# Kernel optimization log

Hardware: AMD Instinct MI355X
Metric: run time of the kernel (lower is better)

The kernel has to match this reference:

```python
import jax, jax.numpy as jnp
import numpy as np

CH, KS, PAD = 64, 3, 1
B, H, W = 4, 128, 128
EH, EW = 64, 64
K = KS * KS


def setup_inputs() -> dict:
    key = jax.random.key(0)
    ks = jax.random.split(key, 10)
    C = CH
    z = lambda *s: jnp.zeros(s, jnp.float32)
    return {
        "ev_feat": jax.random.normal(ks[0], (B, C, EH, EW), jnp.float32),
        "im_feat": jax.random.normal(ks[1], (B, C, H, W), jnp.float32),
        "mlp_w0": jax.random.normal(ks[2], (2 * C + 4, C), jnp.float32) * 0.05,
        "mlp_b0": z(C),
        "mlp_w1": jax.random.normal(ks[3], (C, C), jnp.float32) * 0.05,
        "mlp_b1": z(C),
        "mlp_w2": jax.random.normal(ks[4], (C, C), jnp.float32) * 0.05,
        "mlp_b2": z(C),
        "mlp_w3": jax.random.normal(ks[5], (C, C), jnp.float32) * 0.05,
        "mlp_b3": z(C),
        "off_w": jax.random.normal(ks[6], (3 * K, C, KS, KS), jnp.float32) * 0.01,
        "off_b": z(3 * K),
        "dcn_w": jax.random.normal(ks[7], (C, C, KS, KS), jnp.float32) * 0.05,
        "dcn_b": z(C),
    }


def _conv(x, w, b):
    y = jax.lax.conv_general_dilated(x, w, (1, 1), [(PAD, PAD), (PAD, PAD)],
                                     dimension_numbers=("NCHW", "OIHW", "NCHW"))
    return y + b[None, :, None, None]


def _forward(ev_feat, im_feat, mlp_w0, mlp_b0, mlp_w1, mlp_b1, mlp_w2, mlp_b2,
             mlp_w3, mlp_b3, off_w, off_b, dcn_w, dcn_b):
    C = CH
    Bn = im_feat.shape[0]
    Q = H * W
    # ---- coordinate-conditioned MLP: LIIF-style nearest query of ev_feat ----
    ys = -1.0 + (2.0 * jnp.arange(H, dtype=jnp.float32) + 1.0) / H  # pixel centers in [-1,1]
    xs = -1.0 + (2.0 * jnp.arange(W, dtype=jnp.float32) + 1.0) / W
    gy, gx = jnp.meshgrid(ys, xs, indexing="ij")
    coord = jnp.stack([gy, gx], -1).reshape(-1, 2)  # (Q,2) as (y,x), torch make_coord order
    iy = jnp.clip(jnp.round(((coord[:, 0] + 1.0) * EH - 1.0) / 2.0), 0, EH - 1).astype(jnp.int32)
    ix = jnp.clip(jnp.round(((coord[:, 1] + 1.0) * EW - 1.0) / 2.0), 0, EW - 1).astype(jnp.int32)
    q_feat = ev_feat[:, :, iy, ix].transpose(0, 2, 1)  # (B,Q,C) nearest-sampled event feature
    q_coord = jnp.stack([-1.0 + (2.0 * iy + 1.0) / EH, -1.0 + (2.0 * ix + 1.0) / EW], -1)
    rel = (coord - q_coord) * jnp.array([EH, EW], jnp.float32)  # (Q,2) rel coord scaled by feat res
    rel_cell = jnp.array([2.0 / H * EH, 2.0 / W * EW], jnp.float32)  # cell * feat res
    q_im = im_feat.reshape(Bn, C, Q).transpose(0, 2, 1)  # (B,Q,C); coords are im_feat pixel centers
    inp = jnp.concatenate([q_feat, q_im,
                           jnp.broadcast_to(rel, (Bn, Q, 2)),
                           jnp.broadcast_to(rel_cell, (Bn, Q, 2))], -1)  # (B,Q,2C+4)
    x = jax.nn.relu(inp @ mlp_w0 + mlp_b0)
    x = jax.nn.relu(x @ mlp_w1 + mlp_b1)
    x = jax.nn.relu(x @ mlp_w2 + mlp_b2)
    x = x @ mlp_w3 + mlp_b3  # (B,Q,C)
    feat = x.reshape(Bn, H, W, C).transpose(0, 3, 1, 2)  # (B,C,H,W)
    # ---- ModulatedDeformConvPack (DCNv2) ----
    oo = _conv(feat, off_w, off_b)  # (B,3K,H,W)
    o1, o2, m = oo[:, :K], oo[:, K:2 * K], oo[:, 2 * K:]
    off = jnp.concatenate([o1, o2], 1)  # (B,2K,H,W), interleaved (y,x) per kernel tap
    off_y, off_x = off[:, 0::2], off[:, 1::2]  # (B,K,H,W)
    mask = jax.nn.sigmoid(m)  # (B,K,H,W)
    ky = (jnp.arange(K) // KS - PAD).astype(jnp.float32)
    kx = (jnp.arange(K) % KS - PAD).astype(jnp.float32)
    py = jnp.arange(H, dtype=jnp.float32)[None, :, None] + ky[:, None, None] + off_y  # (B,K,H,W)
    px = jnp.arange(W, dtype=jnp.float32)[None, None, :] + kx[:, None, None] + off_x
    y0 = jnp.floor(py)
    x0 = jnp.floor(px)
    ly = py - y0
    lx = px - x0

    def gather(yi, xi):
        valid = (yi >= 0) & (yi <= H - 1) & (xi >= 0) & (xi <= W - 1)
        yc = jnp.clip(yi, 0, H - 1).astype(jnp.int32)
        xc = jnp.clip(xi, 0, W - 1).astype(jnp.int32)
        v = jax.vmap(lambda img, yy, xx: img[:, yy, xx])(feat, yc, xc)  # (B,C,K,H,W)
        return v * valid[:, None].astype(feat.dtype)

    w00 = ((1 - ly) * (1 - lx))[:, None]
    w01 = ((1 - ly) * lx)[:, None]
    w10 = (ly * (1 - lx))[:, None]
    w11 = (ly * lx)[:, None]
    samp = (gather(y0, x0) * w00 + gather(y0, x0 + 1) * w01 +
            gather(y0 + 1, x0) * w10 + gather(y0 + 1, x0 + 1) * w11)  # (B,C,K,H,W)
    samp = samp * mask[:, None]
    out = jnp.einsum("bckhw,ock->bohw", samp, dcn_w.reshape(C, C, K))
    return out + dcn_b[None, :, None, None]


def reference(ev_feat, im_feat, mlp_w0, mlp_b0, mlp_w1, mlp_b1, mlp_w2, mlp_b2,
              mlp_w3, mlp_b3, off_w, off_b, dcn_w, dcn_b):
    return _forward(ev_feat, im_feat, mlp_w0, mlp_b0, mlp_w1, mlp_b1, mlp_w2, mlp_b2,
                    mlp_w3, mlp_b3, off_w, off_b, dcn_w, dcn_b)
```

## Files before the change

### kernel.cpp

```cpp
#include <hip/hip_runtime.h>
#include <math.h>

#define CCH 64
#define HH  128
#define WW  128
#define NB  4
#define NPIX (NB*HH*WW)
#define NWG  (NPIX/64)

__device__ __forceinline__ int swz_block(int bid) {
    return (bid & 7) * (NWG >> 3) + (bid >> 3);
}

__global__ __launch_bounds__(256) void prep_kernel(
    const float* __restrict__ off_w, const float* __restrict__ dcn_w,
    float* __restrict__ offT, float* __restrict__ dcnT)
{
    int idx = blockIdx.x * 256 + threadIdx.x;
    if (idx < 576 * 28) {
        int rc = idx / 28;
        int o  = idx % 28;
        offT[rc * 28 + o] = (o < 27) ? off_w[o * 576 + rc] : 0.0f;
    }
    if (idx < 36864) {
        int o    = idx & 63;
        int rest = idx >> 6;
        int ic   = rest & 63;
        int k    = rest >> 6;
        dcnT[(k * 64 + ic) * 64 + o] = dcn_w[o * 576 + ic * 9 + k];
    }
}

__global__ __launch_bounds__(256) void mlp_kernel(
    const float* __restrict__ ev, const float* __restrict__ im,
    const float* __restrict__ w0, const float* __restrict__ b0,
    const float* __restrict__ w1, const float* __restrict__ b1,
    const float* __restrict__ w2, const float* __restrict__ b2,
    const float* __restrict__ w3, const float* __restrict__ b3,
    float* __restrict__ feat)
{
    __shared__ float xA[64 * 64];
    __shared__ float xB[64 * 64];
    int tid  = threadIdx.x;
    int cg   = __builtin_amdgcn_readfirstlane(tid >> 6);
    int lane = tid & 63;
    int p = swz_block(blockIdx.x) * 64 + lane;
    int b = p >> 14;
    int q = p & 16383;
    int h = q >> 7;
    int w = q & 127;
    int c0 = cg * 16;

    float acc[16];
#pragma unroll
    for (int j = 0; j < 16; ++j) acc[j] = b0[c0 + j];

    const float* evb = ev + ((b * 64) * 64 + (h >> 1)) * 64 + (w >> 1);
    for (int i = 0; i < 64; ++i) {
        float v = evb[i * 4096];
        const float* wr = w0 + i * 64 + c0;
#pragma unroll
        for (int j = 0; j < 16; ++j) acc[j] = fmaf(v, wr[j], acc[j]);
    }
    const float* imb = im + ((b * 64) * 128 + h) * 128 + w;
    for (int i = 0; i < 64; ++i) {
        float v = imb[i * 16384];
        const float* wr = w0 + (64 + i) * 64 + c0;
#pragma unroll
        for (int j = 0; j < 16; ++j) acc[j] = fmaf(v, wr[j], acc[j]);
    }
    {
        float rely = (h & 1) ? 0.5f : -0.5f;
        float relx = (w & 1) ? 0.5f : -0.5f;
        const float* wr = w0 + 128 * 64 + c0;
#pragma unroll
        for (int j = 0; j < 16; ++j) acc[j] = fmaf(rely, wr[j], acc[j]);
#pragma unroll
        for (int j = 0; j < 16; ++j) acc[j] = fmaf(relx, wr[64 + j], acc[j]);
#pragma unroll
        for (int j = 0; j < 16; ++j) acc[j] += wr[128 + j] + wr[192 + j];
    }
#pragma unroll
    for (int j = 0; j < 16; ++j) xA[(c0 + j) * 64 + lane] = fmaxf(acc[j], 0.0f);
    __syncthreads();

#pragma unroll
    for (int j = 0; j < 16; ++j) acc[j] = b1[c0 + j];
    for (int i = 0; i < 64; ++i) {
        float v = xA[i * 64 + lane];
        const float* wr = w1 + i * 64 + c0;
#pragma unroll
        for (int j = 0; j < 16; ++j) acc[j] = fmaf(v, wr[j], acc[j]);
    }
#pragma unroll
    for (int j = 0; j < 16; ++j) xB[(c0 + j) * 64 + lane] = fmaxf(acc[j], 0.0f);
    __syncthreads();

#pragma unroll
    for (int j = 0; j < 16; ++j) acc[j] = b2[c0 + j];
    for (int i = 0; i < 64; ++i) {
        float v = xB[i * 64 + lane];
        const float* wr = w2 + i * 64 + c0;
#pragma unroll
        for (int j = 0; j < 16; ++j) acc[j] = fmaf(v, wr[j], acc[j]);
    }
#pragma unroll
    for (int j = 0; j < 16; ++j) xA[(c0 + j) * 64 + lane] = fmaxf(acc[j], 0.0f);
    __syncthreads();

#pragma unroll
    for (int j = 0; j < 16; ++j) acc[j] = b3[c0 + j];
    for (int i = 0; i < 64; ++i) {
        float v = xA[i * 64 + lane];
        const float* wr = w3 + i * 64 + c0;
#pragma unroll
        for (int j = 0; j < 16; ++j) acc[j] = fmaf(v, wr[j], acc[j]);
    }
    float* fb = feat + (b * 64 + c0) * 16384 + q;
#pragma unroll
    for (int j = 0; j < 16; ++j) fb[j * 16384] = acc[j];
}

__global__ __launch_bounds__(256) void off_kernel(
    const float* __restrict__ feat, const float* __restrict__ offT,
    const float* __restrict__ off_b,
    float* __restrict__ oo)
{
    __shared__ float po[4 * 27 * 64];
    int tid  = threadIdx.x;
    int wv   = __builtin_amdgcn_readfirstlane(tid >> 6);
    int lane = tid & 63;
    int p = swz_block(blockIdx.x) * 64 + lane;
    int b = p >> 14;
    int q = p & 16383;
    int h = q >> 7;
    int w = q & 127;
    int c0 = wv * 16;

    float acc[27];
#pragma unroll
    for (int o = 0; o < 27; ++o) acc[o] = 0.0f;

    const float* fb = feat + (b * 64 + c0) * 16384;
    for (int i = 0; i < 16; ++i) {
        const float* f = fb + i * 16384;
        float v[9];
#pragma unroll
        for (int ky = 0; ky < 3; ++ky)
#pragma unroll
            for (int kx = 0; kx < 3; ++kx) {
                int y = h + ky - 1, x = w + kx - 1;
                bool ok = (y >= 0) && (y < 128) && (x >= 0) && (x < 128);
                v[ky * 3 + kx] = ok ? f[y * 128 + x] : 0.0f;
            }
#pragma unroll
        for (int kk = 0; kk < 9; ++kk) {
            const float* wr = offT + ((c0 + i) * 9 + kk) * 28;
#pragma unroll
            for (int o = 0; o < 27; ++o) acc[o] = fmaf(v[kk], wr[o], acc[o]);
        }
    }

#pragma unroll
    for (int o = 0; o < 27; ++o) po[(wv * 27 + o) * 64 + lane] = acc[o];
    __syncthreads();

#pragma unroll
    for (int j = 0; j < 7; ++j) {
        int o = wv + 4 * j;
        if (o < 27) {
            float s = off_b[o]
                    + po[o * 64 + lane] + po[(27 + o) * 64 + lane]
                    + po[(54 + o) * 64 + lane] + po[(81 + o) * 64 + lane];
            oo[((b * 27 + o) << 14) + q] = s;
        }
    }
}

__device__ __forceinline__ void dcn_transform(
    const float* oob, int k, int h, int w,
    float& W00, float& W01, float& W10, float& W11,
    int& i00, int& i01, int& i10, int& i11)
{
    float oy = oob[(2 * k) << 14];
    float ox = oob[(2 * k + 1) << 14];
    float ml = 1.0f / (1.0f + expf(-oob[(18 + k) << 14]));
    float py = (float)(h + k / 3 - 1) + oy;
    float px = (float)(w + k % 3 - 1) + ox;

    float y0f = floorf(py), x0f = floorf(px);
    float ly = py - y0f, lx = px - x0f;
    int y0 = (int)y0f, x0 = (int)x0f;

    bool vy0 = (y0f >= 0.0f)        && (y0f <= 127.0f);
    bool vy1 = (y0f + 1.0f >= 0.0f) && (y0f + 1.0f <= 127.0f);
    bool vx0 = (x0f >= 0.0f)        && (x0f <= 127.0f);
    bool vx1 = (x0f + 1.0f >= 0.0f) && (x0f + 1.0f <= 127.0f);

    int yc0 = min(max(y0, 0), 127),     yc1 = min(max(y0 + 1, 0), 127);
    int xc0 = min(max(x0, 0), 127),     xc1 = min(max(x0 + 1, 0), 127);

    W00 = (1.0f - ly) * (1.0f - lx) * ml * ((vy0 && vx0) ? 1.0f : 0.0f);
    W01 = (1.0f - ly) * lx          * ml * ((vy0 && vx1) ? 1.0f : 0.0f);
    W10 = ly * (1.0f - lx)          * ml * ((vy1 && vx0) ? 1.0f : 0.0f);
    W11 = ly * lx                   * ml * ((vy1 && vx1) ? 1.0f : 0.0f);

    i00 = yc0 * 128 + xc0; i01 = yc0 * 128 + xc1;
    i10 = yc1 * 128 + xc0; i11 = yc1 * 128 + xc1;
}

__global__ __launch_bounds__(256) void dcn_kernel(
    const float* __restrict__ feat,
    const float* __restrict__ oo,
    const float* __restrict__ dcnT, const float* __restrict__ dcn_b,
    float* __restrict__ out)
{
    __shared__ float sA[64 * 64];
    __shared__ float sB[64 * 64];
    int tid  = threadIdx.x;
    int wv   = __builtin_amdgcn_readfirstlane(tid >> 6);
    int lane = tid & 63;
    int p = swz_block(blockIdx.x) * 64 + lane;
    int b = p >> 14;
    int q = p & 16383;
    int h = q >> 7;
    int w = q & 127;
    int c0 = wv * 16;

    float acc[16];
#pragma unroll
    for (int j = 0; j < 16; ++j) acc[j] = dcn_b[c0 + j];

    const float* fb  = feat + (b * 64 + c0) * 16384;
    const float* oob = oo + ((b * 27) << 14) + q;

    {
        float W00, W01, W10, W11; int i00, i01, i10, i11;
        dcn_transform(oob, 0, h, w, W00, W01, W10, W11, i00, i01, i10, i11);
#pragma unroll 8
        for (int i = 0; i < 16; ++i) {
            const float* f = fb + i * 16384;
            float s = W00 * f[i00] + W01 * f[i01] + W10 * f[i10] + W11 * f[i11];
            sA[(c0 + i) * 64 + lane] = s;
        }
    }
    __syncthreads();

    float* cur = sA;
    float* nxt = sB;

    for (int k = 0; k < 9; ++k) {
        bool pre = (k < 8);
        float W00, W01, W10, W11; int i00, i01, i10, i11;
        float r00[8], r01[8], r10[8], r11[8];

        if (pre) {
            dcn_transform(oob, k + 1, h, w, W00, W01, W10, W11, i00, i01, i10, i11);
#pragma unroll
            for (int i = 0; i < 8; ++i) {
                const float* f = fb + i * 16384;
                r00[i] = f[i00]; r01[i] = f[i01]; r10[i] = f[i10]; r11[i] = f[i11];
            }
        }

        const float* wk = dcnT + (k * 64) * 64 + c0;
#pragma unroll 8
        for (int ic = 0; ic < 32; ++ic) {
            float s = cur[ic * 64 + lane];
            const float* wr = wk + ic * 64;
#pragma unroll
            for (int j = 0; j < 16; ++j) acc[j] = fmaf(s, wr[j], acc[j]);
        }

        if (pre) {
#pragma unroll
            for (int i = 0; i < 8; ++i)
                nxt[(c0 + i) * 64 + lane] =
                    W00 * r00[i] + W01 * r01[i] + W10 * r10[i] + W11 * r11[i];
#pragma unroll
            for (int i = 0; i < 8; ++i) {
                const float* f = fb + (8 + i) * 16384;
                r00[i] = f[i00]; r01[i] = f[i01]; r10[i] = f[i10]; r11[i] = f[i11];
            }
        }

#pragma unroll 8
        for (int ic = 32; ic < 64; ++ic) {
            float s = cur[ic * 64 + lane];
            const float* wr = wk + ic * 64;
#pragma unroll
            for (int j = 0; j < 16; ++j) acc[j] = fmaf(s, wr[j], acc[j]);
        }

        if (pre) {
#pragma unroll
            for (int i = 0; i < 8; ++i)
                nxt[(c0 + 8 + i) * 64 + lane] =
                    W00 * r00[i] + W01 * r01[i] + W10 * r10[i] + W11 * r11[i];
        }

        __syncthreads();
        float* t = cur; cur = nxt; nxt = t;
    }

    float* ob = out + (b * 64 + c0) * 16384 + q;
#pragma unroll
    for (int j = 0; j < 16; ++j) ob[j * 16384] = acc[j];
}

extern "C" void kernel_launch(void* const* d_in, const int* in_sizes, int n_in,
                              void* d_out, int out_size, void* d_ws, size_t ws_size,
                              hipStream_t stream)
{
    const float* ev    = (const float*)d_in[0];
    const float* im    = (const float*)d_in[1];
    const float* w0    = (const float*)d_in[2];
    const float* b0    = (const float*)d_in[3];
    const float* w1    = (const float*)d_in[4];
    const float* b1    = (const float*)d_in[5];
    const float* w2    = (const float*)d_in[6];
    const float* b2    = (const float*)d_in[7];
    const float* w3    = (const float*)d_in[8];
    const float* b3    = (const float*)d_in[9];
    const float* off_w = (const float*)d_in[10];
    const float* off_b = (const float*)d_in[11];
    const float* dcn_w = (const float*)d_in[12];
    const float* dcn_b = (const float*)d_in[13];
    float* out = (float*)d_out;

    char* ws = (char*)d_ws;
    float* feat  = (float*)(ws);
    float* oo    = (float*)(ws + 16777216);
    float* offT  = (float*)(ws + 23855104);
    float* dcnT  = (float*)(ws + 23920640);

    prep_kernel<<<144, 256, 0, stream>>>(off_w, dcn_w, offT, dcnT);
    mlp_kernel<<<NWG, 256, 0, stream>>>(ev, im, w0, b0, w1, b1, w2, b2,
                                        w3, b3, feat);
    off_kernel<<<NWG, 256, 0, stream>>>(feat, offT, off_b, oo);
    dcn_kernel<<<NWG, 256, 0, stream>>>(feat, oo, dcnT, dcn_b, out);
}
```

Baseline: 182.1 us.

## Store intermediate features channels-last and gather them with float4 loads

The MLP output buffer moves from NCHW to NHWC layout. The offset conv and deformable conv then fetch 16 contiguous channels per sampled pixel with float4 loads instead of 16 strided scalar loads. The aim is fewer memory transactions and better cache-line use in the random bilinear gathers. In exchange, each lane's MLP writes and off-conv reads now stride 256 bytes between neighbouring pixels, so a single warp access is no longer coalesced across lanes.

```diff
diff --git a/kernel.cpp b/kernel.cpp
--- a/kernel.cpp
+++ b/kernel.cpp
@@ -37,7 +37,7 @@
     const float* __restrict__ w1, const float* __restrict__ b1,
     const float* __restrict__ w2, const float* __restrict__ b2,
     const float* __restrict__ w3, const float* __restrict__ b3,
-    float* __restrict__ feat)
+    float* __restrict__ feat2)
 {
     __shared__ float xA[64 * 64];
     __shared__ float xB[64 * 64];
@@ -116,13 +116,14 @@
 #pragma unroll
         for (int j = 0; j < 16; ++j) acc[j] = fmaf(v, wr[j], acc[j]);
     }
-    float* fb = feat + (b * 64 + c0) * 16384 + q;
-#pragma unroll
-    for (int j = 0; j < 16; ++j) fb[j * 16384] = acc[j];
+    float4* f4 = (float4*)(feat2 + ((b * 16384 + q) * 64 + c0));
+#pragma unroll
+    for (int j = 0; j < 4; ++j)
+        f4[j] = make_float4(acc[4 * j], acc[4 * j + 1], acc[4 * j + 2], acc[4 * j + 3]);
 }
 
 __global__ __launch_bounds__(256) void off_kernel(
-    const float* __restrict__ feat, const float* __restrict__ offT,
+    const float* __restrict__ feat2, const float* __restrict__ offT,
     const float* __restrict__ off_b,
     float* __restrict__ oo)
 {
@@ -141,23 +142,24 @@
 #pragma unroll
     for (int o = 0; o < 27; ++o) acc[o] = 0.0f;
 
-    const float* fb = feat + (b * 64 + c0) * 16384;
-    for (int i = 0; i < 16; ++i) {
-        const float* f = fb + i * 16384;
-        float v[9];
-#pragma unroll
-        for (int ky = 0; ky < 3; ++ky)
-#pragma unroll
-            for (int kx = 0; kx < 3; ++kx) {
-                int y = h + ky - 1, x = w + kx - 1;
-                bool ok = (y >= 0) && (y < 128) && (x >= 0) && (x < 128);
-                v[ky * 3 + kx] = ok ? f[y * 128 + x] : 0.0f;
-            }
-#pragma unroll
-        for (int kk = 0; kk < 9; ++kk) {
+    const float* f2 = feat2 + (b * 16384) * 64 + c0;
+#pragma unroll 3
+    for (int kk = 0; kk < 9; ++kk) {
+        int y = h + kk / 3 - 1, x = w + kk % 3 - 1;
+        bool ok = (y >= 0) && (y < 128) && (x >= 0) && (x < 128);
+        int yc = min(max(y, 0), 127), xc = min(max(x, 0), 127);
+        const float4* fp = (const float4*)(f2 + (yc * 128 + xc) * 64);
+        float4 v0 = fp[0], v1 = fp[1], v2 = fp[2], v3 = fp[3];
+        float zz = ok ? 1.0f : 0.0f;
+        float vv[16] = {v0.x*zz, v0.y*zz, v0.z*zz, v0.w*zz,
+                        v1.x*zz, v1.y*zz, v1.z*zz, v1.w*zz,
+                        v2.x*zz, v2.y*zz, v2.z*zz, v2.w*zz,
+                        v3.x*zz, v3.y*zz, v3.z*zz, v3.w*zz};
+#pragma unroll
+        for (int i = 0; i < 16; ++i) {
             const float* wr = offT + ((c0 + i) * 9 + kk) * 28;
 #pragma unroll
-            for (int o = 0; o < 27; ++o) acc[o] = fmaf(v[kk], wr[o], acc[o]);
+            for (int o = 0; o < 27; ++o) acc[o] = fmaf(vv[i], wr[o], acc[o]);
         }
     }
 
@@ -210,7 +212,7 @@
 }
 
 __global__ __launch_bounds__(256) void dcn_kernel(
-    const float* __restrict__ feat,
+    const float* __restrict__ feat2,
     const float* __restrict__ oo,
     const float* __restrict__ dcnT, const float* __restrict__ dcn_b,
     float* __restrict__ out)
@@ -231,17 +233,23 @@
 #pragma unroll
     for (int j = 0; j < 16; ++j) acc[j] = dcn_b[c0 + j];
 
-    const float* fb  = feat + (b * 64 + c0) * 16384;
+    const float* fb2 = feat2 + (b * 16384) * 64 + c0;
     const float* oob = oo + ((b * 27) << 14) + q;
 
     {
         float W00, W01, W10, W11; int i00, i01, i10, i11;
         dcn_transform(oob, 0, h, w, W00, W01, W10, W11, i00, i01, i10, i11);
-#pragma unroll 8
-        for (int i = 0; i < 16; ++i) {
-            const float* f = fb + i * 16384;
-            float s = W00 * f[i00] + W01 * f[i01] + W10 * f[i10] + W11 * f[i11];
-            sA[(c0 + i) * 64 + lane] = s;
+        const float4* p00 = (const float4*)(fb2 + i00 * 64);
+        const float4* p01 = (const float4*)(fb2 + i01 * 64);
+        const float4* p10 = (const float4*)(fb2 + i10 * 64);
+        const float4* p11 = (const float4*)(fb2 + i11 * 64);
+#pragma unroll
+        for (int g = 0; g < 4; ++g) {
+            float4 a = p00[g], bb = p01[g], c = p10[g], d = p11[g];
+            sA[(c0 + 4 * g + 0) * 64 + lane] = W00 * a.x + W01 * bb.x + W10 * c.x + W11 * d.x;
+            sA[(c0 + 4 * g + 1) * 64 + lane] = W00 * a.y + W01 * bb.y + W10 * c.y + W11 * d.y;
+            sA[(c0 + 4 * g + 2) * 64 + lane] = W00 * a.z + W01 * bb.z + W10 * c.z + W11 * d.z;
+            sA[(c0 + 4 * g + 3) * 64 + lane] = W00 * a.w + W01 * bb.w + W10 * c.w + W11 * d.w;
         }
     }
     __syncthreads();
@@ -252,15 +260,19 @@
     for (int k = 0; k < 9; ++k) {
         bool pre = (k < 8);
         float W00, W01, W10, W11; int i00, i01, i10, i11;
-        float r00[8], r01[8], r10[8], r11[8];
+        float4 a0, a1, b0, b1, c0v, c1v, d0, d1;
+        const float4 *p00 = nullptr, *p01 = nullptr, *p10 = nullptr, *p11 = nullptr;
 
         if (pre) {
             dcn_transform(oob, k + 1, h, w, W00, W01, W10, W11, i00, i01, i10, i11);
-#pragma unroll
-            for (int i = 0; i < 8; ++i) {
-                const float* f = fb + i * 16384;
-                r00[i] = f[i00]; r01[i] = f[i01]; r10[i] = f[i10]; r11[i] = f[i11];
-            }
+            p00 = (const float4*)(fb2 + i00 * 64);
+            p01 = (const float4*)(fb2 + i01 * 64);
+            p10 = (const float4*)(fb2 + i10 * 64);
+            p11 = (const float4*)(fb2 + i11 * 64);
+            a0 = p00[0]; a1 = p00[1];
+            b0 = p01[0]; b1 = p01[1];
+            c0v = p10[0]; c1v = p10[1];
+            d0 = p11[0]; d1 = p11[1];
         }
 
         const float* wk = dcnT + (k * 64) * 64 + c0;
@@ -273,15 +285,18 @@
         }
 
         if (pre) {
-#pragma unroll
-            for (int i = 0; i < 8; ++i)
-                nxt[(c0 + i) * 64 + lane] =
-                    W00 * r00[i] + W01 * r01[i] + W10 * r10[i] + W11 * r11[i];
-#pragma unroll
-            for (int i = 0; i < 8; ++i) {
-                const float* f = fb + (8 + i) * 16384;
-                r00[i] = f[i00]; r01[i] = f[i01]; r10[i] = f[i10]; r11[i] = f[i11];
-            }
+            nxt[(c0 + 0) * 64 + lane] = W00 * a0.x + W01 * b0.x + W10 * c0v.x + W11 * d0.x;
+            nxt[(c0 + 1) * 64 + lane] = W00 * a0.y + W01 * b0.y + W10 * c0v.y + W11 * d0.y;
+            nxt[(c0 + 2) * 64 + lane] = W00 * a0.z + W01 * b0.z + W10 * c0v.z + W11 * d0.z;
+            nxt[(c0 + 3) * 64 + lane] = W00 * a0.w + W01 * b0.w + W10 * c0v.w + W11 * d0.w;
+            nxt[(c0 + 4) * 64 + lane] = W00 * a1.x + W01 * b1.x + W10 * c1v.x + W11 * d1.x;
+            nxt[(c0 + 5) * 64 + lane] = W00 * a1.y + W01 * b1.y + W10 * c1v.y + W11 * d1.y;
+            nxt[(c0 + 6) * 64 + lane] = W00 * a1.z + W01 * b1.z + W10 * c1v.z + W11 * d1.z;
+            nxt[(c0 + 7) * 64 + lane] = W00 * a1.w + W01 * b1.w + W10 * c1v.w + W11 * d1.w;
+            a0 = p00[2]; a1 = p00[3];
+            b0 = p01[2]; b1 = p01[3];
+            c0v = p10[2]; c1v = p10[3];
+            d0 = p11[2]; d1 = p11[3];
         }
 
 #pragma unroll 8
@@ -293,10 +308,14 @@
         }
 
         if (pre) {
-#pragma unroll
-            for (int i = 0; i < 8; ++i)
-                nxt[(c0 + 8 + i) * 64 + lane] =
-                    W00 * r00[i] + W01 * r01[i] + W10 * r10[i] + W11 * r11[i];
+            nxt[(c0 +  8) * 64 + lane] = W00 * a0.x + W01 * b0.x + W10 * c0v.x + W11 * d0.x;
+            nxt[(c0 +  9) * 64 + lane] = W00 * a0.y + W01 * b0.y + W10 * c0v.y + W11 * d0.y;
+            nxt[(c0 + 10) * 64 + lane] = W00 * a0.z + W01 * b0.z + W10 * c0v.z + W11 * d0.z;
+            nxt[(c0 + 11) * 64 + lane] = W00 * a0.w + W01 * b0.w + W10 * c0v.w + W11 * d0.w;
+            nxt[(c0 + 12) * 64 + lane] = W00 * a1.x + W01 * b1.x + W10 * c1v.x + W11 * d1.x;
+            nxt[(c0 + 13) * 64 + lane] = W00 * a1.y + W01 * b1.y + W10 * c1v.y + W11 * d1.y;
+            nxt[(c0 + 14) * 64 + lane] = W00 * a1.z + W01 * b1.z + W10 * c1v.z + W11 * d1.z;
+            nxt[(c0 + 15) * 64 + lane] = W00 * a1.w + W01 * b1.w + W10 * c1v.w + W11 * d1.w;
         }
 
         __syncthreads();
@@ -329,14 +348,14 @@
     float* out = (float*)d_out;
 
     char* ws = (char*)d_ws;
-    float* feat  = (float*)(ws);
+    float* feat2 = (float*)(ws);
     float* oo    = (float*)(ws + 16777216);
     float* offT  = (float*)(ws + 23855104);
     float* dcnT  = (float*)(ws + 23920640);
 
     prep_kernel<<<144, 256, 0, stream>>>(off_w, dcn_w, offT, dcnT);
     mlp_kernel<<<NWG, 256, 0, stream>>>(ev, im, w0, b0, w1, b1, w2, b2,
-                                        w3, b3, feat);
-    off_kernel<<<NWG, 256, 0, stream>>>(feat, offT, off_b, oo);
-    dcn_kernel<<<NWG, 256, 0, stream>>>(feat, oo, dcnT, dcn_b, out);
-}
+                                        w3, b3, feat2);
+    off_kernel<<<NWG, 256, 0, stream>>>(feat2, offT, off_b, oo);
+    dcn_kernel<<<NWG, 256, 0, stream>>>(feat2, oo, dcnT, dcn_b, out);
+}
```

After: 184.8 us. No clear change (+1.5%).

## Gather DCN samples from a channel-last feature copy with float4 loads

Applied to the files above, without the earlier changes.

The MLP kernel now also writes a pixel-major (NHWC) copy of the features, transposed through padded shared memory. The deformable-conv kernel gathers each bilinear corner as contiguous float4 channel groups instead of strided per-channel scalar loads. It also runs 512 threads per block with 8 output channels per wave and an XOR-swizzled shared-memory layout. The NCHW copy still feeds the offset conv and is stored temporarily in the output buffer. The cost is an extra 16 MB feature write, plus more weight loads per sample because each wave computes fewer outputs.

```diff
diff --git a/kernel.cpp b/kernel.cpp
--- a/kernel.cpp
+++ b/kernel.cpp
@@ -37,14 +37,15 @@
     const float* __restrict__ w1, const float* __restrict__ b1,
     const float* __restrict__ w2, const float* __restrict__ b2,
     const float* __restrict__ w3, const float* __restrict__ b3,
-    float* __restrict__ feat)
-{
-    __shared__ float xA[64 * 64];
-    __shared__ float xB[64 * 64];
+    float* __restrict__ feat2, float* __restrict__ featN)
+{
+    __shared__ float xA[64 * 65];
+    __shared__ float xB[64 * 65];
     int tid  = threadIdx.x;
     int cg   = __builtin_amdgcn_readfirstlane(tid >> 6);
     int lane = tid & 63;
-    int p = swz_block(blockIdx.x) * 64 + lane;
+    int sw   = swz_block(blockIdx.x);
+    int p = sw * 64 + lane;
     int b = p >> 14;
     int q = p & 16383;
     int h = q >> 7;
@@ -81,48 +82,67 @@
         for (int j = 0; j < 16; ++j) acc[j] += wr[128 + j] + wr[192 + j];
     }
 #pragma unroll
-    for (int j = 0; j < 16; ++j) xA[(c0 + j) * 64 + lane] = fmaxf(acc[j], 0.0f);
+    for (int j = 0; j < 16; ++j) xA[(c0 + j) * 65 + lane] = fmaxf(acc[j], 0.0f);
     __syncthreads();
 
 #pragma unroll
     for (int j = 0; j < 16; ++j) acc[j] = b1[c0 + j];
     for (int i = 0; i < 64; ++i) {
-        float v = xA[i * 64 + lane];
+        float v = xA[i * 65 + lane];
         const float* wr = w1 + i * 64 + c0;
 #pragma unroll
         for (int j = 0; j < 16; ++j) acc[j] = fmaf(v, wr[j], acc[j]);
     }
 #pragma unroll
-    for (int j = 0; j < 16; ++j) xB[(c0 + j) * 64 + lane] = fmaxf(acc[j], 0.0f);
+    for (int j = 0; j < 16; ++j) xB[(c0 + j) * 65 + lane] = fmaxf(acc[j], 0.0f);
     __syncthreads();
 
 #pragma unroll
     for (int j = 0; j < 16; ++j) acc[j] = b2[c0 + j];
     for (int i = 0; i < 64; ++i) {
-        float v = xB[i * 64 + lane];
+        float v = xB[i * 65 + lane];
         const float* wr = w2 + i * 64 + c0;
 #pragma unroll
         for (int j = 0; j < 16; ++j) acc[j] = fmaf(v, wr[j], acc[j]);
     }
 #pragma unroll
-    for (int j = 0; j < 16; ++j) xA[(c0 + j) * 64 + lane] = fmaxf(acc[j], 0.0f);
+    for (int j = 0; j < 16; ++j) xA[(c0 + j) * 65 + lane] = fmaxf(acc[j], 0.0f);
     __syncthreads();
 
 #pragma unroll
     for (int j = 0; j < 16; ++j) acc[j] = b3[c0 + j];
     for (int i = 0; i < 64; ++i) {
-        float v = xA[i * 64 + lane];
+        float v = xA[i * 65 + lane];
         const float* wr = w3 + i * 64 + c0;
 #pragma unroll
         for (int j = 0; j < 16; ++j) acc[j] = fmaf(v, wr[j], acc[j]);
     }
-    float* fb = feat + (b * 64 + c0) * 16384 + q;
-#pragma unroll
-    for (int j = 0; j < 16; ++j) fb[j * 16384] = acc[j];
+
+    float* fbN = featN + (b * 64 + c0) * 16384 + q;
+#pragma unroll
+    for (int j = 0; j < 16; ++j) fbN[j * 16384] = acc[j];
+
+#pragma unroll
+    for (int j = 0; j < 16; ++j) xB[(c0 + j) * 65 + lane] = acc[j];
+    __syncthreads();
+    {
+        int q0 = (sw * 64) & 16383;
+        float* fb = feat2 + ((size_t)b * 16384 + q0) * 64;
+        int ch0 = (tid & 15) * 4;
+#pragma unroll
+        for (int r = 0; r < 4; ++r) {
+            int px = (tid >> 4) + r * 16;
+            float4 v = make_float4(xB[(ch0 + 0) * 65 + px],
+                                   xB[(ch0 + 1) * 65 + px],
+                                   xB[(ch0 + 2) * 65 + px],
+                                   xB[(ch0 + 3) * 65 + px]);
+            ((float4*)fb)[tid + r * 256] = v;
+        }
+    }
 }
 
 __global__ __launch_bounds__(256) void off_kernel(
-    const float* __restrict__ feat, const float* __restrict__ offT,
+    const float* __restrict__ featN, const float* __restrict__ offT,
     const float* __restrict__ off_b,
     float* __restrict__ oo)
 {
@@ -141,7 +161,7 @@
 #pragma unroll
     for (int o = 0; o < 27; ++o) acc[o] = 0.0f;
 
-    const float* fb = feat + (b * 64 + c0) * 16384;
+    const float* fb = featN + (b * 64 + c0) * 16384;
     for (int i = 0; i < 16; ++i) {
         const float* f = fb + i * 16384;
         float v[9];
@@ -209,8 +229,17 @@
     i10 = yc1 * 128 + xc0; i11 = yc1 * 128 + xc1;
 }
 
-__global__ __launch_bounds__(256) void dcn_kernel(
-    const float* __restrict__ feat,
+__device__ __forceinline__ float4 blend4(float W00, float W01, float W10, float W11,
+                                         float4 a, float4 b, float4 c, float4 d)
+{
+    return make_float4(W00*a.x + W01*b.x + W10*c.x + W11*d.x,
+                       W00*a.y + W01*b.y + W10*c.y + W11*d.y,
+                       W00*a.z + W01*b.z + W10*c.z + W11*d.z,
+                       W00*a.w + W01*b.w + W10*c.w + W11*d.w);
+}
+
+__global__ __launch_bounds__(512) void dcn_kernel(
+    const float* __restrict__ feat2,
     const float* __restrict__ oo,
     const float* __restrict__ dcnT, const float* __restrict__ dcn_b,
     float* __restrict__ out)
@@ -225,87 +254,99 @@
     int q = p & 16383;
     int h = q >> 7;
     int w = q & 127;
-    int c0 = wv * 16;
-
-    float acc[16];
-#pragma unroll
-    for (int j = 0; j < 16; ++j) acc[j] = dcn_b[c0 + j];
-
-    const float* fb  = feat + (b * 64 + c0) * 16384;
+    int o0 = wv * 8;
+    int gc = wv * 2;
+    int swz = lane & 15;
+
+    float acc[8];
+#pragma unroll
+    for (int j = 0; j < 8; ++j) acc[j] = dcn_b[o0 + j];
+
+    const float* fb2 = feat2 + (size_t)(b * 16384) * 64;
     const float* oob = oo + ((b * 27) << 14) + q;
+
+    float4* sA4 = (float4*)sA;
+    float4* sB4 = (float4*)sB;
 
     {
         float W00, W01, W10, W11; int i00, i01, i10, i11;
         dcn_transform(oob, 0, h, w, W00, W01, W10, W11, i00, i01, i10, i11);
-#pragma unroll 8
-        for (int i = 0; i < 16; ++i) {
-            const float* f = fb + i * 16384;
-            float s = W00 * f[i00] + W01 * f[i01] + W10 * f[i10] + W11 * f[i11];
-            sA[(c0 + i) * 64 + lane] = s;
-        }
-    }
-    __syncthreads();
-
-    float* cur = sA;
-    float* nxt = sB;
+#pragma unroll
+        for (int c = 0; c < 2; ++c) {
+            int icb = gc + c;
+            float4 a = *(const float4*)(fb2 + i00 * 64 + icb * 4);
+            float4 bb= *(const float4*)(fb2 + i01 * 64 + icb * 4);
+            float4 cc= *(const float4*)(fb2 + i10 * 64 + icb * 4);
+            float4 dd= *(const float4*)(fb2 + i11 * 64 + icb * 4);
+            sA4[lane * 16 + (icb ^ swz)] = blend4(W00, W01, W10, W11, a, bb, cc, dd);
+        }
+    }
+    __syncthreads();
+
+    float4* cur = sA4;
+    float4* nxt = sB4;
 
     for (int k = 0; k < 9; ++k) {
         bool pre = (k < 8);
         float W00, W01, W10, W11; int i00, i01, i10, i11;
-        float r00[8], r01[8], r10[8], r11[8];
+        float4 a0, b0, c0v, d0;
 
         if (pre) {
             dcn_transform(oob, k + 1, h, w, W00, W01, W10, W11, i00, i01, i10, i11);
-#pragma unroll
-            for (int i = 0; i < 8; ++i) {
-                const float* f = fb + i * 16384;
-                r00[i] = f[i00]; r01[i] = f[i01]; r10[i] = f[i10]; r11[i] = f[i11];
-            }
-        }
-
-        const float* wk = dcnT + (k * 64) * 64 + c0;
-#pragma unroll 8
-        for (int ic = 0; ic < 32; ++ic) {
-            float s = cur[ic * 64 + lane];
-            const float* wr = wk + ic * 64;
-#pragma unroll
-            for (int j = 0; j < 16; ++j) acc[j] = fmaf(s, wr[j], acc[j]);
+            a0 = *(const float4*)(fb2 + i00 * 64 + gc * 4);
+            b0 = *(const float4*)(fb2 + i01 * 64 + gc * 4);
+            c0v= *(const float4*)(fb2 + i10 * 64 + gc * 4);
+            d0 = *(const float4*)(fb2 + i11 * 64 + gc * 4);
+        }
+
+        const float* wk = dcnT + k * 4096 + o0;
+#pragma unroll
+        for (int icb = 0; icb < 8; ++icb) {
+            float4 s4 = cur[lane * 16 + (icb ^ swz)];
+            const float* wr = wk + icb * 256;
+#pragma unroll
+            for (int j = 0; j < 8; ++j) acc[j] = fmaf(s4.x, wr[j], acc[j]);
+#pragma unroll
+            for (int j = 0; j < 8; ++j) acc[j] = fmaf(s4.y, wr[64 + j], acc[j]);
+#pragma unroll
+            for (int j = 0; j < 8; ++j) acc[j] = fmaf(s4.z, wr[128 + j], acc[j]);
+#pragma unroll
+            for (int j = 0; j < 8; ++j) acc[j] = fmaf(s4.w, wr[192 + j], acc[j]);
         }
 
         if (pre) {
-#pragma unroll
-            for (int i = 0; i < 8; ++i)
-                nxt[(c0 + i) * 64 + lane] =
-                    W00 * r00[i] + W01 * r01[i] + W10 * r10[i] + W11 * r11[i];
-#pragma unroll
-            for (int i = 0; i < 8; ++i) {
-                const float* f = fb + (8 + i) * 16384;
-                r00[i] = f[i00]; r01[i] = f[i01]; r10[i] = f[i10]; r11[i] = f[i11];
-            }
-        }
-
-#pragma unroll 8
-        for (int ic = 32; ic < 64; ++ic) {
-            float s = cur[ic * 64 + lane];
-            const float* wr = wk + ic * 64;
-#pragma unroll
-            for (int j = 0; j < 16; ++j) acc[j] = fmaf(s, wr[j], acc[j]);
+            nxt[lane * 16 + (gc ^ swz)] = blend4(W00, W01, W10, W11, a0, b0, c0v, d0);
+            a0 = *(const float4*)(fb2 + i00 * 64 + (gc + 1) * 4);
+            b0 = *(const float4*)(fb2 + i01 * 64 + (gc + 1) * 4);
+            c0v= *(const float4*)(fb2 + i10 * 64 + (gc + 1) * 4);
+            d0 = *(const float4*)(fb2 + i11 * 64 + (gc + 1) * 4);
+        }
+
+#pragma unroll
+        for (int icb = 8; icb < 16; ++icb) {
+            float4 s4 = cur[lane * 16 + (icb ^ swz)];
+            const float* wr = wk + icb * 256;
+#pragma unroll
+            for (int j = 0; j < 8; ++j) acc[j] = fmaf(s4.x, wr[j], acc[j]);
+#pragma unroll
+            for (int j = 0; j < 8; ++j) acc[j] = fmaf(s4.y, wr[64 + j], acc[j]);
+#pragma unroll
+            for (int j = 0; j < 8; ++j) acc[j] = fmaf(s4.z, wr[128 + j], acc[j]);
+#pragma unroll
+            for (int j = 0; j < 8; ++j) acc[j] = fmaf(s4.w, wr[192 + j], acc[j]);
         }
 
         if (pre) {
-#pragma unroll
-            for (int i = 0; i < 8; ++i)
-                nxt[(c0 + 8 + i) * 64 + lane] =
-                    W00 * r00[i] + W01 * r01[i] + W10 * r10[i] + W11 * r11[i];
+            nxt[lane * 16 + ((gc + 1) ^ swz)] = blend4(W00, W01, W10, W11, a0, b0, c0v, d0);
         }
 
         __syncthreads();
-        float* t = cur; cur = nxt; nxt = t;
-    }
-
-    float* ob = out + (b * 64 + c0) * 16384 + q;
-#pragma unroll
-    for (int j = 0; j < 16; ++j) ob[j * 16384] = acc[j];
+        float4* t = cur; cur = nxt; nxt = t;
+    }
+
+    float* ob = out + (b * 64 + o0) * 16384 + q;
+#pragma unroll
+    for (int j = 0; j < 8; ++j) ob[j * 16384] = acc[j];
 }
 
 extern "C" void kernel_launch(void* const* d_in, const int* in_sizes, int n_in,
@@ -329,14 +370,15 @@
     float* out = (float*)d_out;
 
     char* ws = (char*)d_ws;
-    float* feat  = (float*)(ws);
+    float* feat2 = (float*)(ws);
     float* oo    = (float*)(ws + 16777216);
     float* offT  = (float*)(ws + 23855104);
     float* dcnT  = (float*)(ws + 23920640);
+    float* featN = out;
 
     prep_kernel<<<144, 256, 0, stream>>>(off_w, dcn_w, offT, dcnT);
     mlp_kernel<<<NWG, 256, 0, stream>>>(ev, im, w0, b0, w1, b1, w2, b2,
-                                        w3, b3, feat);
-    off_kernel<<<NWG, 256, 0, stream>>>(feat, offT, off_b, oo);
-    dcn_kernel<<<NWG, 256, 0, stream>>>(feat, oo, dcnT, dcn_b, out);
-}
+                                        w3, b3, feat2, featN);
+    off_kernel<<<NWG, 256, 0, stream>>>(featN, offT, off_b, oo);
+    dcn_kernel<<<NWG, 512, 0, stream>>>(feat2, oo, dcnT, dcn_b, out);
+}
```

Result: slower. 480.0 us (+163.6%).
